# Performance work log

Hardware: AMD Instinct MI355X
Metric: run time of the kernel (lower is better)

Reference implementation:

```python
import jax, jax.numpy as jnp
import numpy as np

B, N, K = 16, 2048, 16          # clouds, points per cloud, knn k
C_IN, C_OUT = 64, 64

def setup_inputs() -> dict:
    key = jax.random.key(0)
    ks = jax.random.split(key, 8)
    s_in = 1.0 / np.sqrt(C_IN)
    return {
        "x": jax.random.normal(ks[0], (B * N, C_IN), jnp.float32),
        "pos": jax.random.normal(ks[1], (B * N, 3), jnp.float32),
        "batch": jnp.repeat(jnp.arange(B, dtype=jnp.int32), N),
        "W_pos": jax.random.normal(ks[2], (3, C_OUT), jnp.float32) / np.sqrt(3.0),
        "b_pos": jnp.zeros((C_OUT,), jnp.float32),
        "W_attn": jax.random.normal(ks[3], (C_OUT, C_OUT), jnp.float32) / np.sqrt(C_OUT),
        "b_attn": jnp.zeros((C_OUT,), jnp.float32),
        "W_val": jax.random.normal(ks[4], (C_IN, C_OUT), jnp.float32) * s_in,
        "W_src": jax.random.normal(ks[5], (C_IN, C_OUT), jnp.float32) * s_in,
        "W_dst": jax.random.normal(ks[6], (C_IN, C_OUT), jnp.float32) * s_in,
    }

def _gather(a, idx):
    # a: [B, N, D], idx: [B, N, K+1] -> [B, N, K+1, D]
    return jax.vmap(lambda ab, ib: ab[ib])(a, idx)

def reference(x, pos, batch, W_pos, b_pos, W_attn, b_attn, W_val, W_src, W_dst):
    # batch is assumed contiguous with equal-size clouds (B clouds of N points),
    # so batch-restricted knn_graph == per-cloud knn after reshape.
    posr = pos.reshape(B, N, 3)
    xr = x.reshape(B, N, C_IN)
    # knn_graph(loop=False): exclude self, then PointTransformerConv re-adds self loops
    d2 = jnp.sum((posr[:, :, None, :] - posr[:, None, :, :]) ** 2, axis=-1)  # [B,N,N]
    d2 = d2 + jnp.eye(N, dtype=d2.dtype) * 1e10
    _, nbr = jax.lax.top_k(-d2, K)                                # [B,N,K] sources j per target i
    self_idx = jnp.broadcast_to(jnp.arange(N)[None, :, None], (B, N, 1))
    nbr = jnp.concatenate([nbr, self_idx], axis=2)                # self loop -> [B,N,K+1]
    alpha_i = xr @ W_dst                                          # lin_dst(x_i)  [B,N,C_OUT]
    alpha_j = _gather(xr @ W_src, nbr)                            # lin_src(x_j)  [B,N,K+1,C_OUT]
    val_j = _gather(xr @ W_val, nbr)                              # lin(x_j)
    pos_j = _gather(posr, nbr)                                    # [B,N,K+1,3]
    delta = (posr[:, :, None, :] - pos_j) @ W_pos + b_pos         # pos_nn(pos_i - pos_j)
    alpha = alpha_i[:, :, None, :] - alpha_j + delta              # subtraction attention
    alpha = alpha @ W_attn + b_attn                               # attn_nn
    alpha = jax.nn.softmax(alpha, axis=2)                         # segment softmax per target i
    out = jnp.sum(alpha * (val_j + delta), axis=2)                # weighted scatter-sum
    return out.reshape(B * N, C_OUT)
```

## Files before the change

kernel.cpp:

```cpp
#include <hip/hip_runtime.h>
#include <math.h>

#define BBATCH 16
#define NPC    2048
#define KNBR   16
#define NPTS   (BBATCH*NPC)
#define NGEMM  512
#define NKNN   512
#define BUFCAP 512

__global__ __launch_bounds__(1024) void prep_kernel(
    const float* __restrict__ Wpos, const float* __restrict__ bpos,
    const float* __restrict__ Wattn, const float* __restrict__ battn,
    const float* __restrict__ Wsrc, const float* __restrict__ Wdst,
    float* __restrict__ Hd, float* __restrict__ Hs,
    float* __restrict__ WP2, float* __restrict__ bb) {
  __shared__ float sW[4096];
  __shared__ float sD[4096];
  __shared__ float sS[4096];
  int t = threadIdx.x;
  ((float4*)sW)[t] = ((const float4*)Wattn)[t];
  ((float4*)sD)[t] = ((const float4*)Wdst)[t];
  ((float4*)sS)[t] = ((const float4*)Wsrc)[t];
  __syncthreads();
  int c = t & 63, r0 = t >> 6;
#pragma unroll
  for (int q = 0; q < 4; ++q) {
    int r = r0 + 16 * q;
    float ad = 0.f, as = 0.f;
    for (int d = 0; d < 64; ++d) {
      float w = sW[d * 64 + c];
      ad += sD[r * 64 + d] * w;
      as += sS[r * 64 + d] * w;
    }
    Hd[r * 64 + c] = ad;
    Hs[r * 64 + c] = as;
  }
  if (t < 64) {
    for (int rr = 0; rr < 3; ++rr) {
      float a = 0.f;
      for (int d = 0; d < 64; ++d) a += Wpos[rr * 64 + d] * sW[d * 64 + t];
      WP2[rr * 64 + t] = a;
    }
    float a = battn[t];
    for (int d = 0; d < 64; ++d) a += bpos[d] * sW[d * 64 + t];
    bb[t] = a;
  }
}

__global__ __launch_bounds__(1024) void fused_gk_kernel(
    const float* __restrict__ pos, const float* __restrict__ x,
    const float* __restrict__ Hd, const float* __restrict__ Hs,
    const float* __restrict__ Wval,
    int* __restrict__ nbr, float* __restrict__ A2, float* __restrict__ S2,
    float* __restrict__ V) {
  __shared__ __align__(16) char smem[65536];
  int t = threadIdx.x;
  int bid = blockIdx.x;
  int c = t & 63, g = t >> 6;

  if (bid < NGEMM) {
    float* R0 = (float*)smem;
    float* R1 = (float*)(smem + 16384);
    float* R2 = (float*)(smem + 32768);
    float* R3 = (float*)(smem + 49152);
    ((float4*)R0)[t] = ((const float4*)(x + (size_t)bid * 64 * 64))[t];
    ((float4*)R1)[t] = ((const float4*)Hd)[t];
    ((float4*)R2)[t] = ((const float4*)Hs)[t];
    ((float4*)R3)[t] = ((const float4*)Wval)[t];
    __syncthreads();

    float v0 = 0, v1 = 0, v2 = 0, v3 = 0;
    float a0 = 0, a1 = 0, a2 = 0, a3 = 0;
    float s0 = 0, s1 = 0, s2 = 0, s3 = 0;
    const float4* xr0 = (const float4*)(R0 + (g * 4 + 0) * 64);
    const float4* xr1 = (const float4*)(R0 + (g * 4 + 1) * 64);
    const float4* xr2 = (const float4*)(R0 + (g * 4 + 2) * 64);
    const float4* xr3 = (const float4*)(R0 + (g * 4 + 3) * 64);
#pragma unroll 4
    for (int k4 = 0; k4 < 16; ++k4) {
      float4 q0 = xr0[k4], q1 = xr1[k4], q2 = xr2[k4], q3 = xr3[k4];
#pragma unroll
      for (int kk = 0; kk < 4; ++kk) {
        int k = k4 * 4 + kk;
        float wv = R3[k * 64 + c];
        float wa = R1[k * 64 + c];
        float ws = R2[k * 64 + c];
        float e0 = (kk == 0) ? q0.x : (kk == 1) ? q0.y : (kk == 2) ? q0.z : q0.w;
        float e1 = (kk == 0) ? q1.x : (kk == 1) ? q1.y : (kk == 2) ? q1.z : q1.w;
        float e2 = (kk == 0) ? q2.x : (kk == 1) ? q2.y : (kk == 2) ? q2.z : q2.w;
        float e3 = (kk == 0) ? q3.x : (kk == 1) ? q3.y : (kk == 2) ? q3.z : q3.w;
        v0 += e0 * wv; v1 += e1 * wv; v2 += e2 * wv; v3 += e3 * wv;
        a0 += e0 * wa; a1 += e1 * wa; a2 += e2 * wa; a3 += e3 * wa;
        s0 += e0 * ws; s1 += e1 * ws; s2 += e2 * ws; s3 += e3 * ws;
      }
    }
    size_t o0 = ((size_t)bid * 64 + g * 4 + 0) * 64 + c;
    V[o0] = v0; A2[o0] = a0; S2[o0] = s0;
    size_t o1 = o0 + 64;  V[o1] = v1; A2[o1] = a1; S2[o1] = s1;
    size_t o2 = o0 + 128; V[o2] = v2; A2[o2] = a2; S2[o2] = s2;
    size_t o3 = o0 + 192; V[o3] = v3; A2[o3] = a3; S2[o3] = s3;
    return;
  }

  int kb = bid - NGEMM;
  float4* pos4 = (float4*)smem;
  unsigned short* buf = (unsigned short*)(smem + 32768);
  int cloud = kb >> 5;
  const float* pc = pos + (size_t)cloud * NPC * 3;
  for (int p = t; p < NPC; p += 1024)
    pos4[p] = make_float4(pc[3 * p], pc[3 * p + 1], pc[3 * p + 2], 0.f);
  __syncthreads();

  int w = g, lane = c;
  for (int u = 0; u < 4; ++u) {
    int lt = u * 16 + w;
    int gi = kb * 64 + lt;
    int ti = gi & (NPC - 1);
    float4 tp = pos4[ti];
    float tx = tp.x, ty = tp.y, tz = tp.z;

    int bkt[32];
#pragma unroll
    for (int cc = 0; cc < 32; ++cc) {
      int j = cc * 64 + lane;
      float4 q = pos4[j];
      float dx = tx - q.x, dy = ty - q.y, dz = tz - q.z;
      float d2 = dx * dx + dy * dy + dz * dz;
      int b = (int)(__float_as_uint(d2) >> 20) - 896;
      bkt[cc] = max(0, min(255, b));
    }

    int lo = 0, hi = 255;
    for (int it = 0; it < 8; ++it) {
      int mid = (lo + hi) >> 1;
      int cnt = 0;
#pragma unroll
      for (int cc = 0; cc < 32; ++cc)
        cnt += (int)__popcll(__ballot(bkt[cc] <= mid));
      if (cnt >= 17) hi = mid; else lo = mid + 1;
    }
    int Tp1 = min(hi + 1, 255);

    int base = 0;
#pragma unroll
    for (int cc = 0; cc < 32; ++cc) {
      bool f = (bkt[cc] <= Tp1);
      unsigned long long mm = __ballot(f);
      unsigned int pre = __builtin_amdgcn_mbcnt_hi(
          (unsigned)(mm >> 32), __builtin_amdgcn_mbcnt_lo((unsigned)mm, 0u));
      if (f) {
        int p = base + (int)pre;
        if (p < BUFCAP) buf[w * BUFCAP + p] = (unsigned short)(cc * 64 + lane);
      }
      base += (int)__popcll(mm);
    }
    int n = min(base, BUFCAP);
    double txd = (double)tx, tyd = (double)ty, tzd = (double)tz;

    if (n <= 64) {
      unsigned long long gb = 0xFFFFFFFFFFFFFFFFull;
      int gj = 0x40000000 + lane;
      if (lane < n) {
        int j = buf[w * BUFCAP + lane];
        if (j != ti) {
          float4 q = pos4[j];
          double dx = __dsub_rn(txd, (double)q.x);
          double dy = __dsub_rn(tyd, (double)q.y);
          double dz = __dsub_rn(tzd, (double)q.z);
          double d2 = __dadd_rn(__dadd_rn(__dmul_rn(dx, dx), __dmul_rn(dy, dy)),
                                __dmul_rn(dz, dz));
          gb = (unsigned long long)__double_as_longlong(d2);
          gj = j;
        }
      }
      for (int k = 2; k <= 64; k <<= 1) {
        for (int jj = k >> 1; jj > 0; jj >>= 1) {
          unsigned long long ob = __shfl_xor(gb, jj);
          int oj = __shfl_xor(gj, jj);
          bool keepmin = (((lane & k) == 0) == ((lane & jj) == 0));
          bool less = (ob < gb) || (ob == gb && oj < gj);
          if (keepmin == less) { gb = ob; gj = oj; }
        }
      }
      if (lane < KNBR) nbr[(size_t)gi * KNBR + lane] = gj;
    } else {
      unsigned long long kb2[8];
      int id2[8];
#pragma unroll
      for (int r = 0; r < 8; ++r) {
        int e = r * 64 + lane;
        kb2[r] = 0xFFFFFFFFFFFFFFFFull;
        id2[r] = 0x40000000 + e;
        if (e < n) {
          int j = buf[w * BUFCAP + e];
          if (j != ti) {
            float4 q = pos4[j];
            double dx = __dsub_rn(txd, (double)q.x);
            double dy = __dsub_rn(tyd, (double)q.y);
            double dz = __dsub_rn(tzd, (double)q.z);
            double d2 = __dadd_rn(
                __dadd_rn(__dmul_rn(dx, dx), __dmul_rn(dy, dy)),
                __dmul_rn(dz, dz));
            kb2[r] = (unsigned long long)__double_as_longlong(d2);
            id2[r] = j;
          }
        }
      }
      for (int r = 0; r < KNBR; ++r) {
        unsigned long long lb = kb2[0];
        int lj = id2[0];
#pragma unroll
        for (int cc = 1; cc < 8; ++cc)
          if (kb2[cc] < lb || (kb2[cc] == lb && id2[cc] < lj)) {
            lb = kb2[cc]; lj = id2[cc];
          }
        unsigned long long gb2 = lb;
        int gj2 = lj;
#pragma unroll
        for (int d = 32; d >= 1; d >>= 1) {
          unsigned long long ob = __shfl_xor(gb2, d);
          int oj = __shfl_xor(gj2, d);
          if (ob < gb2 || (ob == gb2 && oj < gj2)) { gb2 = ob; gj2 = oj; }
        }
#pragma unroll
        for (int cc = 0; cc < 8; ++cc)
          if (id2[cc] == gj2) kb2[cc] = 0xFFFFFFFFFFFFFFFFull;
        if (lane == 0) nbr[(size_t)gi * KNBR + r] = gj2;
      }
    }
  }
}

__global__ __launch_bounds__(512) void edge_kernel(
    const float* __restrict__ pos, const int* __restrict__ nbr,
    const float* __restrict__ A2, const float* __restrict__ S2,
    const float* __restrict__ V, const float* __restrict__ WP2,
    const float* __restrict__ bbv, const float* __restrict__ Wpos,
    const float* __restrict__ bpos, float* __restrict__ out) {
  __shared__ float lp[NPC * 3];
  int t = threadIdx.x;
  int bid = blockIdx.x;
  int cloud = bid >> 6;
  int tb = (bid & 63) * 32;
  const float4* pc4 = (const float4*)(pos + (size_t)cloud * NPC * 3);
#pragma unroll
  for (int r = 0; r < 3; ++r) ((float4*)lp)[t + 512 * r] = pc4[t + 512 * r];
  __syncthreads();

  int w = t >> 6, c = t & 63;
  float wp0 = WP2[c], wp1 = WP2[64 + c], wp2 = WP2[128 + c], bbc = bbv[c];
  float u0 = Wpos[c], u1 = Wpos[64 + c], u2 = Wpos[128 + c], bpc = bpos[c];
  size_t cbase = (size_t)cloud * NPC;

  for (int u = 0; u < 4; ++u) {
    int ti = tb + u * 8 + w;
    size_t gi = cbase + ti;
    int jv = nbr[gi * KNBR + (c & 15)];
    float pix = lp[3 * ti], piy = lp[3 * ti + 1], piz = lp[3 * ti + 2];
    float a2 = A2[gi * 64 + c];

    float m = -1e30f, den = 0.f, acc = 0.f;
#pragma unroll
    for (int e = 0; e < 17; ++e) {
      int j = (e < 16) ? __shfl(jv, e) : ti;
      float dx = pix - lp[3 * j];
      float dy = piy - lp[3 * j + 1];
      float dz = piz - lp[3 * j + 2];
      size_t jg = cbase + j;
      float s2 = S2[jg * 64 + c];
      float v = V[jg * 64 + c];
      float lg = a2 - s2 + dx * wp0 + dy * wp1 + dz * wp2 + bbc;
      float vl = v + dx * u0 + dy * u1 + dz * u2 + bpc;
      float mn = fmaxf(m, lg);
      float sc = __expf(m - mn);
      float wgt = __expf(lg - mn);
      den = den * sc + wgt;
      acc = acc * sc + wgt * vl;
      m = mn;
    }
    out[gi * 64 + c] = acc / den;
  }
}

extern "C" void kernel_launch(void* const* d_in, const int* in_sizes, int n_in,
                              void* d_out, int out_size, void* d_ws, size_t ws_size,
                              hipStream_t stream) {
  const float* x     = (const float*)d_in[0];
  const float* pos   = (const float*)d_in[1];
  const float* Wpos  = (const float*)d_in[3];
  const float* bpos  = (const float*)d_in[4];
  const float* Wattn = (const float*)d_in[5];
  const float* battn = (const float*)d_in[6];
  const float* Wval  = (const float*)d_in[7];
  const float* Wsrc  = (const float*)d_in[8];
  const float* Wdst  = (const float*)d_in[9];

  float* ws  = (float*)d_ws;
  float* A2  = ws;
  float* S2  = A2 + (size_t)NPTS * 64;
  float* V   = S2 + (size_t)NPTS * 64;
  float* WP2 = V + (size_t)NPTS * 64;
  float* bb  = WP2 + 192;
  int*   nbr = (int*)(bb + 64);
  float* Hd  = (float*)(nbr + (size_t)NPTS * KNBR);
  float* Hs  = Hd + 4096;
  float* out = (float*)d_out;

  prep_kernel<<<1, 1024, 0, stream>>>(Wpos, bpos, Wattn, battn, Wsrc, Wdst,
                                      Hd, Hs, WP2, bb);
  fused_gk_kernel<<<NGEMM + NKNN, 1024, 0, stream>>>(
      pos, x, Hd, Hs, Wval, nbr, A2, S2, V);
  edge_kernel<<<NPTS / 32, 512, 0, stream>>>(pos, nbr, A2, S2, V, WP2, bb,
                                             Wpos, bpos, out);
}
```

Before: 226.4 us.

## Fuse kNN selection with edge attention, split GEMM into its own kernel

```diff
diff --git a/kernel.cpp b/kernel.cpp
--- a/kernel.cpp
+++ b/kernel.cpp
@@ -48,62 +48,68 @@
   }
 }
 
-__global__ __launch_bounds__(1024) void fused_gk_kernel(
-    const float* __restrict__ pos, const float* __restrict__ x,
-    const float* __restrict__ Hd, const float* __restrict__ Hs,
-    const float* __restrict__ Wval,
-    int* __restrict__ nbr, float* __restrict__ A2, float* __restrict__ S2,
-    float* __restrict__ V) {
-  __shared__ __align__(16) char smem[65536];
+__global__ __launch_bounds__(1024) void gemm_kernel(
+    const float* __restrict__ x, const float* __restrict__ Hd,
+    const float* __restrict__ Hs, const float* __restrict__ Wval,
+    float* __restrict__ A2, float* __restrict__ S2, float* __restrict__ V) {
+  __shared__ __align__(16) float smem[16384];
   int t = threadIdx.x;
   int bid = blockIdx.x;
   int c = t & 63, g = t >> 6;
 
-  if (bid < NGEMM) {
-    float* R0 = (float*)smem;
-    float* R1 = (float*)(smem + 16384);
-    float* R2 = (float*)(smem + 32768);
-    float* R3 = (float*)(smem + 49152);
-    ((float4*)R0)[t] = ((const float4*)(x + (size_t)bid * 64 * 64))[t];
-    ((float4*)R1)[t] = ((const float4*)Hd)[t];
-    ((float4*)R2)[t] = ((const float4*)Hs)[t];
-    ((float4*)R3)[t] = ((const float4*)Wval)[t];
-    __syncthreads();
-
-    float v0 = 0, v1 = 0, v2 = 0, v3 = 0;
-    float a0 = 0, a1 = 0, a2 = 0, a3 = 0;
-    float s0 = 0, s1 = 0, s2 = 0, s3 = 0;
-    const float4* xr0 = (const float4*)(R0 + (g * 4 + 0) * 64);
-    const float4* xr1 = (const float4*)(R0 + (g * 4 + 1) * 64);
-    const float4* xr2 = (const float4*)(R0 + (g * 4 + 2) * 64);
-    const float4* xr3 = (const float4*)(R0 + (g * 4 + 3) * 64);
+  float* R0 = smem;
+  float* R1 = smem + 4096;
+  float* R2 = smem + 8192;
+  float* R3 = smem + 12288;
+  ((float4*)R0)[t] = ((const float4*)(x + (size_t)bid * 64 * 64))[t];
+  ((float4*)R1)[t] = ((const float4*)Hd)[t];
+  ((float4*)R2)[t] = ((const float4*)Hs)[t];
+  ((float4*)R3)[t] = ((const float4*)Wval)[t];
+  __syncthreads();
+
+  float v0 = 0, v1 = 0, v2 = 0, v3 = 0;
+  float a0 = 0, a1 = 0, a2 = 0, a3 = 0;
+  float s0 = 0, s1 = 0, s2 = 0, s3 = 0;
+  const float4* xr0 = (const float4*)(R0 + (g * 4 + 0) * 64);
+  const float4* xr1 = (const float4*)(R0 + (g * 4 + 1) * 64);
+  const float4* xr2 = (const float4*)(R0 + (g * 4 + 2) * 64);
+  const float4* xr3 = (const float4*)(R0 + (g * 4 + 3) * 64);
 #pragma unroll 4
-    for (int k4 = 0; k4 < 16; ++k4) {
-      float4 q0 = xr0[k4], q1 = xr1[k4], q2 = xr2[k4], q3 = xr3[k4];
-#pragma unroll
-      for (int kk = 0; kk < 4; ++kk) {
-        int k = k4 * 4 + kk;
-        float wv = R3[k * 64 + c];
-        float wa = R1[k * 64 + c];
-        float ws = R2[k * 64 + c];
-        float e0 = (kk == 0) ? q0.x : (kk == 1) ? q0.y : (kk == 2) ? q0.z : q0.w;
-        float e1 = (kk == 0) ? q1.x : (kk == 1) ? q1.y : (kk == 2) ? q1.z : q1.w;
-        float e2 = (kk == 0) ? q2.x : (kk == 1) ? q2.y : (kk == 2) ? q2.z : q2.w;
-        float e3 = (kk == 0) ? q3.x : (kk == 1) ? q3.y : (kk == 2) ? q3.z : q3.w;
-        v0 += e0 * wv; v1 += e1 * wv; v2 += e2 * wv; v3 += e3 * wv;
-        a0 += e0 * wa; a1 += e1 * wa; a2 += e2 * wa; a3 += e3 * wa;
-        s0 += e0 * ws; s1 += e1 * ws; s2 += e2 * ws; s3 += e3 * ws;
-      }
-    }
-    size_t o0 = ((size_t)bid * 64 + g * 4 + 0) * 64 + c;
-    V[o0] = v0; A2[o0] = a0; S2[o0] = s0;
-    size_t o1 = o0 + 64;  V[o1] = v1; A2[o1] = a1; S2[o1] = s1;
-    size_t o2 = o0 + 128; V[o2] = v2; A2[o2] = a2; S2[o2] = s2;
-    size_t o3 = o0 + 192; V[o3] = v3; A2[o3] = a3; S2[o3] = s3;
-    return;
-  }
-
-  int kb = bid - NGEMM;
+  for (int k4 = 0; k4 < 16; ++k4) {
+    float4 q0 = xr0[k4], q1 = xr1[k4], q2 = xr2[k4], q3 = xr3[k4];
+#pragma unroll
+    for (int kk = 0; kk < 4; ++kk) {
+      int k = k4 * 4 + kk;
+      float wv = R3[k * 64 + c];
+      float wa = R1[k * 64 + c];
+      float ws = R2[k * 64 + c];
+      float e0 = (kk == 0) ? q0.x : (kk == 1) ? q0.y : (kk == 2) ? q0.z : q0.w;
+      float e1 = (kk == 0) ? q1.x : (kk == 1) ? q1.y : (kk == 2) ? q1.z : q1.w;
+      float e2 = (kk == 0) ? q2.x : (kk == 1) ? q2.y : (kk == 2) ? q2.z : q2.w;
+      float e3 = (kk == 0) ? q3.x : (kk == 1) ? q3.y : (kk == 2) ? q3.z : q3.w;
+      v0 += e0 * wv; v1 += e1 * wv; v2 += e2 * wv; v3 += e3 * wv;
+      a0 += e0 * wa; a1 += e1 * wa; a2 += e2 * wa; a3 += e3 * wa;
+      s0 += e0 * ws; s1 += e1 * ws; s2 += e2 * ws; s3 += e3 * ws;
+    }
+  }
+  size_t o0 = ((size_t)bid * 64 + g * 4 + 0) * 64 + c;
+  V[o0] = v0; A2[o0] = a0; S2[o0] = s0;
+  size_t o1 = o0 + 64;  V[o1] = v1; A2[o1] = a1; S2[o1] = s1;
+  size_t o2 = o0 + 128; V[o2] = v2; A2[o2] = a2; S2[o2] = s2;
+  size_t o3 = o0 + 192; V[o3] = v3; A2[o3] = a3; S2[o3] = s3;
+}
+
+__global__ __launch_bounds__(1024) void knn_edge_kernel(
+    const float* __restrict__ pos, const float* __restrict__ A2,
+    const float* __restrict__ S2, const float* __restrict__ V,
+    const float* __restrict__ WP2, const float* __restrict__ bbv,
+    const float* __restrict__ Wpos, const float* __restrict__ bpos,
+    float* __restrict__ out) {
+  __shared__ __align__(16) char smem[49152];
+  int t = threadIdx.x;
+  int kb = blockIdx.x;
+  int c = t & 63, g = t >> 6;
+
   float4* pos4 = (float4*)smem;
   unsigned short* buf = (unsigned short*)(smem + 32768);
   int cloud = kb >> 5;
@@ -158,6 +164,7 @@
     int n = min(base, BUFCAP);
     double txd = (double)tx, tyd = (double)ty, tzd = (double)tz;
 
+    int jv;
     if (n <= 64) {
       unsigned long long gb = 0xFFFFFFFFFFFFFFFFull;
       int gj = 0x40000000 + lane;
@@ -183,7 +190,7 @@
           if (keepmin == less) { gb = ob; gj = oj; }
         }
       }
-      if (lane < KNBR) nbr[(size_t)gi * KNBR + lane] = gj;
+      jv = gj;
     } else {
       unsigned long long kb2[8];
       int id2[8];
@@ -207,6 +214,7 @@
           }
         }
       }
+      jv = 0;
       for (int r = 0; r < KNBR; ++r) {
         unsigned long long lb = kb2[0];
         int lj = id2[0];
@@ -226,60 +234,37 @@
 #pragma unroll
         for (int cc = 0; cc < 8; ++cc)
           if (id2[cc] == gj2) kb2[cc] = 0xFFFFFFFFFFFFFFFFull;
-        if (lane == 0) nbr[(size_t)gi * KNBR + r] = gj2;
-      }
-    }
-  }
-}
-
-__global__ __launch_bounds__(512) void edge_kernel(
-    const float* __restrict__ pos, const int* __restrict__ nbr,
-    const float* __restrict__ A2, const float* __restrict__ S2,
-    const float* __restrict__ V, const float* __restrict__ WP2,
-    const float* __restrict__ bbv, const float* __restrict__ Wpos,
-    const float* __restrict__ bpos, float* __restrict__ out) {
-  __shared__ float lp[NPC * 3];
-  int t = threadIdx.x;
-  int bid = blockIdx.x;
-  int cloud = bid >> 6;
-  int tb = (bid & 63) * 32;
-  const float4* pc4 = (const float4*)(pos + (size_t)cloud * NPC * 3);
-#pragma unroll
-  for (int r = 0; r < 3; ++r) ((float4*)lp)[t + 512 * r] = pc4[t + 512 * r];
-  __syncthreads();
-
-  int w = t >> 6, c = t & 63;
-  float wp0 = WP2[c], wp1 = WP2[64 + c], wp2 = WP2[128 + c], bbc = bbv[c];
-  float u0 = Wpos[c], u1 = Wpos[64 + c], u2 = Wpos[128 + c], bpc = bpos[c];
-  size_t cbase = (size_t)cloud * NPC;
-
-  for (int u = 0; u < 4; ++u) {
-    int ti = tb + u * 8 + w;
-    size_t gi = cbase + ti;
-    int jv = nbr[gi * KNBR + (c & 15)];
-    float pix = lp[3 * ti], piy = lp[3 * ti + 1], piz = lp[3 * ti + 2];
-    float a2 = A2[gi * 64 + c];
-
-    float m = -1e30f, den = 0.f, acc = 0.f;
-#pragma unroll
-    for (int e = 0; e < 17; ++e) {
-      int j = (e < 16) ? __shfl(jv, e) : ti;
-      float dx = pix - lp[3 * j];
-      float dy = piy - lp[3 * j + 1];
-      float dz = piz - lp[3 * j + 2];
-      size_t jg = cbase + j;
-      float s2 = S2[jg * 64 + c];
-      float v = V[jg * 64 + c];
-      float lg = a2 - s2 + dx * wp0 + dy * wp1 + dz * wp2 + bbc;
-      float vl = v + dx * u0 + dy * u1 + dz * u2 + bpc;
-      float mn = fmaxf(m, lg);
-      float sc = __expf(m - mn);
-      float wgt = __expf(lg - mn);
-      den = den * sc + wgt;
-      acc = acc * sc + wgt * vl;
-      m = mn;
-    }
-    out[gi * 64 + c] = acc / den;
+        if (lane == r) jv = gj2;
+      }
+    }
+
+    {
+      size_t cbase = (size_t)cloud * NPC;
+      float a2v = A2[((size_t)gi) * 64 + lane];
+      float wp0 = WP2[lane], wp1 = WP2[64 + lane], wp2 = WP2[128 + lane];
+      float bbc = bbv[lane];
+      float u0 = Wpos[lane], u1 = Wpos[64 + lane], u2 = Wpos[128 + lane];
+      float bpc = bpos[lane];
+      float m = -1e30f, den = 0.f, acc = 0.f;
+#pragma unroll
+      for (int e = 0; e < 17; ++e) {
+        int j = (e < 16) ? __shfl(jv, e) : ti;
+        float4 q = pos4[j];
+        float dx = tx - q.x, dy = ty - q.y, dz = tz - q.z;
+        size_t jrow = (cbase + j) * 64 + lane;
+        float s2 = S2[jrow];
+        float v = V[jrow];
+        float lg = a2v - s2 + dx * wp0 + dy * wp1 + dz * wp2 + bbc;
+        float vl = v + dx * u0 + dy * u1 + dz * u2 + bpc;
+        float mn = fmaxf(m, lg);
+        float sc = __expf(m - mn);
+        float wgt = __expf(lg - mn);
+        den = den * sc + wgt;
+        acc = acc * sc + wgt * vl;
+        m = mn;
+      }
+      out[((size_t)gi) * 64 + lane] = acc / den;
+    }
   }
 }
 
@@ -302,15 +287,13 @@
   float* V   = S2 + (size_t)NPTS * 64;
   float* WP2 = V + (size_t)NPTS * 64;
   float* bb  = WP2 + 192;
-  int*   nbr = (int*)(bb + 64);
-  float* Hd  = (float*)(nbr + (size_t)NPTS * KNBR);
+  float* Hd  = bb + 64;
   float* Hs  = Hd + 4096;
   float* out = (float*)d_out;
 
   prep_kernel<<<1, 1024, 0, stream>>>(Wpos, bpos, Wattn, battn, Wsrc, Wdst,
                                       Hd, Hs, WP2, bb);
-  fused_gk_kernel<<<NGEMM + NKNN, 1024, 0, stream>>>(
-      pos, x, Hd, Hs, Wval, nbr, A2, S2, V);
-  edge_kernel<<<NPTS / 32, 512, 0, stream>>>(pos, nbr, A2, S2, V, WP2, bb,
+  gemm_kernel<<<NGEMM, 1024, 0, stream>>>(x, Hd, Hs, Wval, A2, S2, V);
+  knn_edge_kernel<<<NKNN, 1024, 0, stream>>>(pos, A2, S2, V, WP2, bb,
                                              Wpos, bpos, out);
 }
```

Result: faster. 209.0 us (-7.7%).
